# Kernel optimization log

Hardware: AMD Instinct MI355X
Metric: run time of the kernel (lower is better)

Reference implementation:

```python
import jax, jax.numpy as jnp
import numpy as np
import math

B, N, R = 1024, 50, 1000
N_POIS = 50000
D = 128
K_T = 64
K_D = 64
T_MAX = 10080.0
D_MAX = 200.0
EARTH_RADIUS_KM = 6371.0
DEG2RAD = math.pi / 180.0


def _interp_scalar(table, x):
    # Linear interpolation into 1-D table [K]; x are bin positions in [0, K-1].
    K = table.shape[0]
    x = jnp.clip(x, 0.0, K - 1 - 1e-06)
    k = jnp.floor(x).astype(jnp.int32)
    frac = x - k.astype(x.dtype)
    return (1.0 - frac) * table[k] + frac * table[jnp.minimum(k + 1, K - 1)]


def _haversine_km(lat1, lon1, lat2, lon2):
    dlat = (lat2 - lat1) * DEG2RAD
    dlon = (lon2 - lon1) * DEG2RAD
    a = jnp.sin(dlat / 2) ** 2 + jnp.cos(lat1 * DEG2RAD) * jnp.cos(lat2 * DEG2RAD) * jnp.sin(dlon / 2) ** 2
    a = jnp.clip(a, 0.0, 1.0)
    return EARTH_RADIUS_KM * 2.0 * jnp.arcsin(jnp.sqrt(a))


def setup_inputs() -> dict:
    key = jax.random.key(0)
    ks = jax.random.split(key, 16)
    poi_idx = jax.random.randint(ks[0], (B, N), 0, N_POIS)
    hour_of_week = jax.random.randint(ks[1], (B, N), 0, 169)
    lat = jax.random.uniform(ks[2], (B, N), jnp.float32)  # ~1 degree spread => up to ~150 km pairwise
    lon = jax.random.uniform(ks[3], (B, N), jnp.float32)
    t_min = jax.random.uniform(ks[4], (B, N), jnp.float32) * T_MAX
    region_centroids = jax.random.uniform(ks[5], (R, 2), jnp.float32)
    poi_emb = 0.02 * jax.random.normal(ks[6], (N_POIS + 1, D), jnp.float32)
    poi_emb = poi_emb.at[N_POIS].set(0.0)  # padding row
    time_emb = 0.02 * jax.random.normal(ks[7], (169, D), jnp.float32)
    time_emb = time_emb.at[0].set(0.0)  # padding row
    E_t = 0.1 * jax.random.normal(ks[8], (K_T,), jnp.float32)
    E_d = 0.1 * jax.random.normal(ks[9], (K_D,), jnp.float32)
    E_d_match = 0.1 * jax.random.normal(ks[10], (K_D,), jnp.float32)
    region_emb = 0.02 * jax.random.normal(ks[11], (R, D), jnp.float32)
    Wq = jax.random.normal(ks[12], (D, D), jnp.float32) / math.sqrt(D)
    Wk = jax.random.normal(ks[13], (D, D), jnp.float32) / math.sqrt(D)
    Wv = jax.random.normal(ks[14], (D, D), jnp.float32) / math.sqrt(D)
    return dict(poi_idx=poi_idx, hour_of_week=hour_of_week, lat=lat, lon=lon, t_min=t_min,
                region_centroids=region_centroids, poi_emb=poi_emb, time_emb=time_emb,
                E_t=E_t, E_d=E_d, E_d_match=E_d_match, region_emb=region_emb,
                Wq=Wq, Wk=Wk, Wv=Wv)


def reference(poi_idx, hour_of_week, lat, lon, t_min, region_centroids,
              poi_emb, time_emb, E_t, E_d, E_d_match, region_emb, Wq, Wk, Wv):
    pad_mask = poi_idx < 0  # [B, n]
    poi_safe = jnp.where(pad_mask, N_POIS, poi_idx)
    hour_safe = jnp.where(pad_mask, 0, hour_of_week)
    x = poi_emb[poi_safe] + time_emb[hour_safe]  # [B, n, D]

    # pairwise trajectory intervals [B, n, n]
    dt = jnp.abs(t_min[:, :, None] - t_min[:, None, :])
    dd = _haversine_km(lat[:, :, None], lon[:, :, None], lat[:, None, :], lon[:, None, :])
    valid = (~pad_mask).astype(x.dtype)
    valid_pair = valid[:, :, None] * valid[:, None, :]
    dt = dt * valid_pair
    dd = dd * valid_pair

    # _PairwiseBias: scalar table interpolation bias
    t_bin = jnp.clip(dt, 0.0, T_MAX) / T_MAX * (K_T - 1)
    d_bin = jnp.clip(dd, 0.0, D_MAX) / D_MAX * (K_D - 1)
    bias = _interp_scalar(E_t, t_bin) + _interp_scalar(E_d, d_bin)  # [B, n, n]

    # _SelfAttn (single head, no LN/residual, dropout=0)
    Q = x @ Wq.T
    K_ = x @ Wk.T
    V = x @ Wv.T
    scores = jnp.einsum('bnd,bmd->bnm', Q, K_) / math.sqrt(D) + bias
    scores = jnp.where(pad_mask[:, None, :], -jnp.inf, scores)
    attn = jnp.nan_to_num(jax.nn.softmax(scores, axis=-1), nan=0.0)
    S = attn @ V  # [B, n, D]

    # _MatchingLayer
    cand_lat = region_centroids[:, 0]
    cand_lon = region_centroids[:, 1]
    dd_m = _haversine_km(lat[:, :, None], lon[:, :, None], cand_lat[None, None, :], cand_lon[None, None, :])  # [B, n, R]
    dbin_m = jnp.clip(dd_m, 0.0, D_MAX) / D_MAX * (K_D - 1)
    bias_match = _interp_scalar(E_d_match, dbin_m)
    m_scores = jnp.einsum('bnd,rd->bnr', S, region_emb) / math.sqrt(D) + bias_match
    m_scores = jnp.where(pad_mask[:, :, None], -jnp.inf, m_scores)
    m_attn = jnp.nan_to_num(jax.nn.softmax(m_scores, axis=1), nan=0.0)  # softmax over trajectory dim
    scores_safe = jnp.where(pad_mask[:, :, None], 0.0, m_scores)
    return jnp.sum(m_attn * scores_safe, axis=1)  # [B, R]
```

## Files before the change

### kernel.cpp

```cpp
#include <hip/hip_runtime.h>
#include <hip/hip_bf16.h>
#include <math.h>

constexpr int BB    = 1024;
constexpr int NN    = 50;
constexpr int RR    = 1000;
constexpr int DD    = 128;
constexpr int NPOIS = 50000;
#define DEG2RADF  0.017453292519943295f
#define KHALF     0.008726646259971648f
#define RSQRTD    0.08838834764831845f
#define DBIN_C0   4013.7373f
#define DBIN_C1   668.95621f
#define TBIN_SC   0.00625f
#define PENAL     -1.0e30f

typedef __attribute__((ext_vector_type(8))) short bfrag8;
typedef __attribute__((ext_vector_type(4))) float f32x4;

__device__ __forceinline__ int swz128(int row, int k) {
    return row * 128 + ((((k) >> 3) ^ (row & 7)) << 3) + (k & 7);
}
__device__ __forceinline__ int swz64(int row, int k) {
    return row * 64 + ((((k) >> 3) ^ (row & 7)) << 3) + (k & 7);
}

__device__ __forceinline__ unsigned short f2bf(float x) {
    union { __hip_bfloat16 h; unsigned short u; } cv;
    cv.h = __float2bfloat16(x);
    return cv.u;
}

__device__ __forceinline__ float cos_small(float x) {
    float x2 = x * x;
    return 1.0f - 0.5f * x2 + 0.041666667f * x2 * x2;
}

__global__ void prep_mg(const float* __restrict__ Wq, const float* __restrict__ Wk,
                        const float* __restrict__ Wv, const float* __restrict__ Re,
                        unsigned short* __restrict__ Mt, unsigned short* __restrict__ G) {
    int k = threadIdx.x;
    if (blockIdx.x < DD) {
        int c = blockIdx.x;
        float s0 = 0.f, s1 = 0.f, s2 = 0.f, s3 = 0.f;
        for (int d = 0; d < DD; d += 4) {
            s0 += Wq[(d + 0) * DD + k] * Wk[(d + 0) * DD + c];
            s1 += Wq[(d + 1) * DD + k] * Wk[(d + 1) * DD + c];
            s2 += Wq[(d + 2) * DD + k] * Wk[(d + 2) * DD + c];
            s3 += Wq[(d + 3) * DD + k] * Wk[(d + 3) * DD + c];
        }
        Mt[c * DD + k] = f2bf((s0 + s1 + s2 + s3) * RSQRTD);
    } else {
        int r = blockIdx.x - DD;
        float s0 = 0.f, s1 = 0.f, s2 = 0.f, s3 = 0.f;
        for (int d = 0; d < DD; d += 4) {
            s0 += Wv[(d + 0) * DD + k] * Re[r * DD + d + 0];
            s1 += Wv[(d + 1) * DD + k] * Re[r * DD + d + 1];
            s2 += Wv[(d + 2) * DD + k] * Re[r * DD + d + 2];
            s3 += Wv[(d + 3) * DD + k] * Re[r * DD + d + 3];
        }
        G[r * DD + k] = f2bf((s0 + s1 + s2 + s3) * RSQRTD);
    }
}

__global__ __launch_bounds__(256) void stan_attn(
    const int* __restrict__ poi_idx, const int* __restrict__ hourw,
    const float* __restrict__ lat, const float* __restrict__ lon,
    const float* __restrict__ tmin,
    const float* __restrict__ poi_emb, const float* __restrict__ time_emb,
    const float* __restrict__ Et_g, const float* __restrict__ Ed_g,
    const unsigned short* __restrict__ Mtb, unsigned short* __restrict__ Zw) {
    __shared__ short xs[64 * 128];
    __shared__ union {
        short ys[64 * 128];
        short ps[64 * 64];
    } u2;
    __shared__ float2 Et2[64], Ed2[64];
    __shared__ float4 bnfo[64];
    __shared__ float  jpen[64];

    const int b = blockIdx.x, tid = threadIdx.x;
    const int wid = tid >> 6, lane = tid & 63;
    const int quad = lane >> 4, colr = lane & 15;

    if (tid < 64) {
        int kk = tid > 62 ? 62 : tid;
        Et2[tid] = make_float2(Et_g[kk], Et_g[kk + 1]);
        Ed2[tid] = make_float2(Ed_g[kk], Ed_g[kk + 1]);
        if (tid < NN) {
            int p = poi_idx[b * NN + tid];
            float la = lat[b * NN + tid], lo = lon[b * NN + tid];
            bnfo[tid] = make_float4(la * KHALF, lo * KHALF,
                                    cos_small(la * DEG2RADF),
                                    tmin[b * NN + tid] * TBIN_SC);
            jpen[tid] = (p < 0) ? PENAL : 0.f;
        } else {
            bnfo[tid] = make_float4(0.f, 0.f, 1.f, 0.f);
            jpen[tid] = PENAL;
        }
    }
    __syncthreads();

    for (int idx = tid; idx < 64 * 64; idx += 256) {
        int n = idx >> 6, c2 = idx & 63;
        float2 v = make_float2(0.f, 0.f);
        if (n < NN) {
            int p = poi_idx[b * NN + n];
            int pd = (p < 0);
            int ps_ = pd ? NPOIS : p;
            int hs  = pd ? 0 : hourw[b * NN + n];
            float2 pe = ((const float2*)(poi_emb  + (size_t)ps_ * DD))[c2];
            float2 te = ((const float2*)(time_emb + (size_t)hs  * DD))[c2];
            v = make_float2(pe.x + te.x, pe.y + te.y);
        }
        unsigned pack = (unsigned)f2bf(v.x) | ((unsigned)f2bf(v.y) << 16);
        ((unsigned*)xs)[n * 64 + (((c2 >> 2) ^ (n & 7)) << 2) + (c2 & 3)] = pack;
    }
    __syncthreads();

    {
        f32x4 accY[2][4];
        #pragma unroll
        for (int ct = 0; ct < 2; ct++)
            #pragma unroll
            for (int mt = 0; mt < 4; mt++) accY[ct][mt] = (f32x4){0.f, 0.f, 0.f, 0.f};
        #pragma unroll
        for (int ks = 0; ks < 4; ks++) {
            const int k0 = ks * 32 + quad * 8;
            bfrag8 av[4], bv[2];
            #pragma unroll
            for (int mt = 0; mt < 4; mt++)
                av[mt] = *(const bfrag8*)(&xs[swz128(mt * 16 + colr, k0)]);
            #pragma unroll
            for (int ct = 0; ct < 2; ct++) {
                int c = wid * 32 + ct * 16 + colr;
                bv[ct] = *(const bfrag8*)(Mtb + (size_t)c * DD + k0);
            }
            #pragma unroll
            for (int ct = 0; ct < 2; ct++)
                #pragma unroll
                for (int mt = 0; mt < 4; mt++)
                    accY[ct][mt] = __builtin_amdgcn_mfma_f32_16x16x32_bf16(
                        av[mt], bv[ct], accY[ct][mt], 0, 0, 0);
        }
        #pragma unroll
        for (int ct = 0; ct < 2; ct++)
            #pragma unroll
            for (int mt = 0; mt < 4; mt++)
                #pragma unroll
                for (int reg = 0; reg < 4; reg++) {
                    int m = mt * 16 + quad * 4 + reg;
                    int c = wid * 32 + ct * 16 + colr;
                    u2.ys[swz128(m, c)] = (short)f2bf(accY[ct][mt][reg]);
                }
    }
    __syncthreads();

    const int i = wid * 16 + colr;
    f32x4 accS[4];
    #pragma unroll
    for (int mt = 0; mt < 4; mt++) accS[mt] = (f32x4){0.f, 0.f, 0.f, 0.f};
    #pragma unroll
    for (int ks = 0; ks < 4; ks++) {
        const int k0 = ks * 32 + quad * 8;
        bfrag8 bv = *(const bfrag8*)(&u2.ys[swz128(i, k0)]);
        #pragma unroll
        for (int mt = 0; mt < 4; mt++) {
            bfrag8 av = *(const bfrag8*)(&xs[swz128(mt * 16 + colr, k0)]);
            accS[mt] = __builtin_amdgcn_mfma_f32_16x16x32_bf16(
                av, bv, accS[mt], 0, 0, 0);
        }
    }
    __syncthreads();

    {
        const float4 bi = bnfo[i];
        float sv[16];
        #pragma unroll
        for (int mt = 0; mt < 4; mt++) {
            #pragma unroll
            for (int reg = 0; reg < 4; reg++) {
                int j = mt * 16 + quad * 4 + reg;
                float4 bj = bnfo[j];
                float tb = fabsf(bi.w - bj.w);
                int   kt = (int)tb;
                float ft = tb - (float)kt;
                float2 et = Et2[kt];
                float bt = fmaf(ft, et.y - et.x, et.x);
                float du = bi.x - bj.x, dv = bi.y - bj.y;
                float a = fmaf((bi.z * bj.z) * dv, dv, du * du);
                float x = __builtin_amdgcn_sqrtf(a);
                float db = x * fmaf(a, DBIN_C1, DBIN_C0);
                int   kd = (int)db;
                float fd = db - (float)kd;
                float2 ed = Ed2[kd];
                float bd = fmaf(fd, ed.y - ed.x, ed.x);
                sv[mt * 4 + reg] = (accS[mt][reg] + bt) + (bd + jpen[j]);
            }
        }
        float mx = sv[0];
        #pragma unroll
        for (int t = 1; t < 16; t++) mx = fmaxf(mx, sv[t]);
        mx = fmaxf(mx, __shfl_xor(mx, 16, 64));
        mx = fmaxf(mx, __shfl_xor(mx, 32, 64));
        float l = 0.f;
        #pragma unroll
        for (int t = 0; t < 16; t++) {
            float p = __expf(sv[t] - mx);
            sv[t] = p;
            l += p;
        }
        l += __shfl_xor(l, 16, 64);
        l += __shfl_xor(l, 32, 64);
        float rl = __builtin_amdgcn_rcpf(l);
        #pragma unroll
        for (int mt = 0; mt < 4; mt++)
            #pragma unroll
            for (int rp = 0; rp < 2; rp++) {
                int j0 = mt * 16 + quad * 4 + rp * 2;
                unsigned lo = f2bf(sv[mt * 4 + rp * 2]     * rl);
                unsigned hi = f2bf(sv[mt * 4 + rp * 2 + 1] * rl);
                ((unsigned*)u2.ps)[i * 32 + (((j0 >> 3) ^ (i & 7)) << 2) + ((j0 & 7) >> 1)]
                    = lo | (hi << 16);
            }
    }
    __syncthreads();

    {
        f32x4 accZ[2][4];
        #pragma unroll
        for (int nt = 0; nt < 2; nt++)
            #pragma unroll
            for (int mt = 0; mt < 4; mt++) accZ[nt][mt] = (f32x4){0.f, 0.f, 0.f, 0.f};
        union BF { unsigned u[4]; bfrag8 v; };
        #pragma unroll
        for (int ks = 0; ks < 2; ks++) {
            const int k0 = ks * 32 + quad * 8;
            bfrag8 av[4];
            #pragma unroll
            for (int mt = 0; mt < 4; mt++)
                av[mt] = *(const bfrag8*)(&u2.ps[swz64(mt * 16 + colr, k0)]);
            BF bvx[2];
            #pragma unroll
            for (int nt = 0; nt < 2; nt++) {
                int d = wid * 32 + nt * 16 + colr;
                #pragma unroll
                for (int t2 = 0; t2 < 4; t2++) {
                    unsigned lo = (unsigned short)xs[swz128(k0 + 2 * t2,     d)];
                    unsigned hi = (unsigned short)xs[swz128(k0 + 2 * t2 + 1, d)];
                    bvx[nt].u[t2] = lo | (hi << 16);
                }
            }
            #pragma unroll
            for (int nt = 0; nt < 2; nt++)
                #pragma unroll
                for (int mt = 0; mt < 4; mt++)
                    accZ[nt][mt] = __builtin_amdgcn_mfma_f32_16x16x32_bf16(
                        av[mt], bvx[nt].v, accZ[nt][mt], 0, 0, 0);
        }
        unsigned short* Zb = Zw + (size_t)b * NN * DD;
        #pragma unroll
        for (int mt = 0; mt < 4; mt++)
            #pragma unroll
            for (int reg = 0; reg < 4; reg++) {
                int ii = mt * 16 + quad * 4 + reg;
                if (ii < NN) {
                    #pragma unroll
                    for (int nt = 0; nt < 2; nt++) {
                        int d = wid * 32 + nt * 16 + colr;
                        Zb[(size_t)ii * DD + d] = f2bf(accZ[nt][mt][reg]);
                    }
                }
            }
    }
}

__global__ __launch_bounds__(256) void stan_match(
    const unsigned short* __restrict__ Zw, const unsigned short* __restrict__ G,
    const float* __restrict__ cent, const float* __restrict__ Em_g,
    const int* __restrict__ poi_idx,
    const float* __restrict__ lat, const float* __restrict__ lon,
    float* __restrict__ out) {
    __shared__ short  As[64 * 128];
    __shared__ short  Bs[64 * 128];
    __shared__ float2 Em2[64];
    __shared__ float4 Rnfo[64];
    __shared__ float4 bnfo[64];

    const int tid = threadIdx.x;
    const int b = blockIdx.x, rt = blockIdx.y;
    const int rbase = rt * 64;

    if (tid < 64) {
        int kk = tid > 62 ? 62 : tid;
        Em2[tid] = make_float2(Em_g[kk], Em_g[kk + 1]);
        int rc = rbase + tid; if (rc > RR - 1) rc = RR - 1;
        float la = cent[rc * 2], lo = cent[rc * 2 + 1];
        Rnfo[tid] = make_float4(la * KHALF, lo * KHALF, cos_small(la * DEG2RADF), 0.f);
        if (tid < NN) {
            float bla = lat[b * NN + tid], blo = lon[b * NN + tid];
            float pen = (poi_idx[b * NN + tid] < 0) ? PENAL : 0.f;
            bnfo[tid] = make_float4(bla * KHALF, blo * KHALF,
                                    cos_small(bla * DEG2RADF), pen);
        } else {
            bnfo[tid] = make_float4(0.f, 0.f, 1.f, PENAL);
        }
    }
    {
        const int row = tid >> 2;
        uint4 z4 = make_uint4(0, 0, 0, 0);
        uint4 a0 = z4, a1 = z4, a2 = z4, a3 = z4;
        if (row < NN) {
            const uint4* src = (const uint4*)(Zw + (size_t)b * NN * DD + row * DD
                                              + (tid & 3) * 32);
            a0 = src[0]; a1 = src[1]; a2 = src[2]; a3 = src[3];
        }
        const int jb = (tid & 3) * 4, rx = row & 7;
        uint4* dstA = (uint4*)As;
        dstA[row * 16 + ((jb + 0) ^ rx)] = a0;
        dstA[row * 16 + ((jb + 1) ^ rx)] = a1;
        dstA[row * 16 + ((jb + 2) ^ rx)] = a2;
        dstA[row * 16 + ((jb + 3) ^ rx)] = a3;
        int gr = rbase + row; if (gr > RR - 1) gr = RR - 1;
        const uint4* srcB = (const uint4*)(G + (size_t)gr * DD + (tid & 3) * 32);
        uint4* dstB = (uint4*)Bs;
        dstB[row * 16 + ((jb + 0) ^ rx)] = srcB[0];
        dstB[row * 16 + ((jb + 1) ^ rx)] = srcB[1];
        dstB[row * 16 + ((jb + 2) ^ rx)] = srcB[2];
        dstB[row * 16 + ((jb + 3) ^ rx)] = srcB[3];
    }
    __syncthreads();

    const int wid  = tid >> 6, lane = tid & 63;
    const int quad = lane >> 4, colr = lane & 15;
    const int rL   = wid * 16 + colr;
    const int r    = rbase + rL;

    f32x4 acc[4];
    #pragma unroll
    for (int mt = 0; mt < 4; mt++) acc[mt] = (f32x4){0.f, 0.f, 0.f, 0.f};

    #pragma unroll
    for (int ks = 0; ks < 4; ks++) {
        const int k0 = ks * 32 + quad * 8;
        bfrag8 bf = *(const bfrag8*)(&Bs[swz128(rL, k0)]);
        #pragma unroll
        for (int mt = 0; mt < 4; mt++) {
            bfrag8 af = *(const bfrag8*)(&As[swz128(mt * 16 + colr, k0)]);
            acc[mt] = __builtin_amdgcn_mfma_f32_16x16x32_bf16(af, bf, acc[mt], 0, 0, 0);
        }
    }

    const float4 rv = Rnfo[rL];
    float s[16];
    #pragma unroll
    for (int mt = 0; mt < 4; mt++) {
        #pragma unroll
        for (int reg = 0; reg < 4; reg++) {
            int n = mt * 16 + quad * 4 + reg;
            float4 bn = bnfo[n];
            float du = bn.x - rv.x, dv = bn.y - rv.y;
            float a = fmaf((bn.z * rv.z) * dv, dv, du * du);
            float x = __builtin_amdgcn_sqrtf(a);
            float db = x * fmaf(a, DBIN_C1, DBIN_C0);
            int   kd = (int)db;
            float fd = db - (float)kd;
            float2 ed = Em2[kd];
            float bias = fmaf(fd, ed.y - ed.x, ed.x);
            s[mt * 4 + reg] = (acc[mt][reg] + bias) + bn.w;
        }
    }
    float m = s[0];
    #pragma unroll
    for (int t = 1; t < 16; t++) m = fmaxf(m, s[t]);
    m = fmaxf(m, __shfl_xor(m, 16, 64));
    m = fmaxf(m, __shfl_xor(m, 32, 64));
    float l = 0.f, a = 0.f;
    #pragma unroll
    for (int t = 0; t < 16; t++) {
        float p = __expf(s[t] - m);
        l += p;
        a = fmaf(p, s[t], a);
    }
    l += __shfl_xor(l, 16, 64); a += __shfl_xor(a, 16, 64);
    l += __shfl_xor(l, 32, 64); a += __shfl_xor(a, 32, 64);
    if (quad == 0 && r < RR)
        out[(size_t)b * RR + r] = a * __builtin_amdgcn_rcpf(l);
}

extern "C" void kernel_launch(void* const* d_in, const int* in_sizes, int n_in,
                              void* d_out, int out_size, void* d_ws, size_t ws_size,
                              hipStream_t stream) {
    const int*   poi_idx  = (const int*)d_in[0];
    const int*   hourw    = (const int*)d_in[1];
    const float* lat      = (const float*)d_in[2];
    const float* lon      = (const float*)d_in[3];
    const float* tmin     = (const float*)d_in[4];
    const float* cent     = (const float*)d_in[5];
    const float* poi_emb  = (const float*)d_in[6];
    const float* time_emb = (const float*)d_in[7];
    const float* E_t      = (const float*)d_in[8];
    const float* E_d      = (const float*)d_in[9];
    const float* E_dm     = (const float*)d_in[10];
    const float* Remb     = (const float*)d_in[11];
    const float* Wq       = (const float*)d_in[12];
    const float* Wk       = (const float*)d_in[13];
    const float* Wv       = (const float*)d_in[14];
    float* out            = (float*)d_out;

    unsigned short* Mtb = (unsigned short*)d_ws;
    unsigned short* Gb  = Mtb + DD * DD;
    unsigned short* Zw  = Gb + (size_t)RR * DD;

    prep_mg<<<dim3(DD + RR), DD, 0, stream>>>(Wq, Wk, Wv, Remb, Mtb, Gb);
    stan_attn<<<dim3(BB), 256, 0, stream>>>(poi_idx, hourw, lat, lon, tmin,
                                            poi_emb, time_emb, E_t, E_d, Mtb, Zw);
    stan_match<<<dim3(BB, 16), 256, 0, stream>>>(Zw, Gb, cent, E_dm, poi_idx, lat, lon, out);
}
```

Before: 189.3 us.

## Fuse attention and matching kernels with double-buffered G tiles and bpermute lookups

Merges the attention kernel and the matching kernel into one kernel per batch. The per-batch Z tile now stays in shared memory instead of round-tripping through global workspace. Inside, the kernel loops over all 16 region tiles, double-buffering the G rows with register prefetch. The E_t/E_d/E_dm table lookups are replaced with cross-lane ds_bpermute from per-lane registers instead of LDS tables. The trade-off is far less grid parallelism (1024 blocks instead of 1024x16) and a serialized loop over region tiles, plus larger LDS use that may lower occupancy.

```diff
diff --git a/kernel.cpp b/kernel.cpp
--- a/kernel.cpp
+++ b/kernel.cpp
@@ -36,6 +36,14 @@
     return 1.0f - 0.5f * x2 + 0.041666667f * x2 * x2;
 }
 
+__device__ __forceinline__ float interp_bp(float eA, float eB, float pos) {
+    int   k = (int)pos;
+    float f = pos - (float)k;
+    float lo = __int_as_float(__builtin_amdgcn_ds_bpermute(k << 2, __float_as_int(eA)));
+    float hi = __int_as_float(__builtin_amdgcn_ds_bpermute(k << 2, __float_as_int(eB)));
+    return fmaf(f, hi - lo, lo);
+}
+
 __global__ void prep_mg(const float* __restrict__ Wq, const float* __restrict__ Wk,
                         const float* __restrict__ Wv, const float* __restrict__ Re,
                         unsigned short* __restrict__ Mt, unsigned short* __restrict__ G) {
@@ -63,19 +71,21 @@
     }
 }
 
-__global__ __launch_bounds__(256) void stan_attn(
+__global__ __launch_bounds__(256) void stan_fused(
     const int* __restrict__ poi_idx, const int* __restrict__ hourw,
     const float* __restrict__ lat, const float* __restrict__ lon,
     const float* __restrict__ tmin,
     const float* __restrict__ poi_emb, const float* __restrict__ time_emb,
     const float* __restrict__ Et_g, const float* __restrict__ Ed_g,
-    const unsigned short* __restrict__ Mtb, unsigned short* __restrict__ Zw) {
+    const float* __restrict__ Em_g, const float* __restrict__ cent,
+    const unsigned short* __restrict__ Mtb, const unsigned short* __restrict__ G,
+    float* __restrict__ out) {
     __shared__ short xs[64 * 128];
     __shared__ union {
         short ys[64 * 128];
         short ps[64 * 64];
     } u2;
-    __shared__ float2 Et2[64], Ed2[64];
+    __shared__ short Bs[2][64 * 128];
     __shared__ float4 bnfo[64];
     __shared__ float  jpen[64];
 
@@ -83,10 +93,12 @@
     const int wid = tid >> 6, lane = tid & 63;
     const int quad = lane >> 4, colr = lane & 15;
 
+    const int lp1 = lane < 63 ? lane + 1 : 63;
+    const float etA = Et_g[lane], etB = Et_g[lp1];
+    const float edA = Ed_g[lane], edB = Ed_g[lp1];
+    const float emA = Em_g[lane], emB = Em_g[lp1];
+
     if (tid < 64) {
-        int kk = tid > 62 ? 62 : tid;
-        Et2[tid] = make_float2(Et_g[kk], Et_g[kk + 1]);
-        Ed2[tid] = make_float2(Ed_g[kk], Ed_g[kk + 1]);
         if (tid < NN) {
             int p = poi_idx[b * NN + tid];
             float la = lat[b * NN + tid], lo = lon[b * NN + tid];
@@ -182,19 +194,11 @@
             for (int reg = 0; reg < 4; reg++) {
                 int j = mt * 16 + quad * 4 + reg;
                 float4 bj = bnfo[j];
-                float tb = fabsf(bi.w - bj.w);
-                int   kt = (int)tb;
-                float ft = tb - (float)kt;
-                float2 et = Et2[kt];
-                float bt = fmaf(ft, et.y - et.x, et.x);
+                float bt = interp_bp(etA, etB, fabsf(bi.w - bj.w));
                 float du = bi.x - bj.x, dv = bi.y - bj.y;
                 float a = fmaf((bi.z * bj.z) * dv, dv, du * du);
                 float x = __builtin_amdgcn_sqrtf(a);
-                float db = x * fmaf(a, DBIN_C1, DBIN_C0);
-                int   kd = (int)db;
-                float fd = db - (float)kd;
-                float2 ed = Ed2[kd];
-                float bd = fmaf(fd, ed.y - ed.x, ed.x);
+                float bd = interp_bp(edA, edB, x * fmaf(a, DBIN_C1, DBIN_C0));
                 sv[mt * 4 + reg] = (accS[mt][reg] + bt) + (bd + jpen[j]);
             }
         }
@@ -226,12 +230,12 @@
     }
     __syncthreads();
 
-    {
-        f32x4 accZ[2][4];
-        #pragma unroll
-        for (int nt = 0; nt < 2; nt++)
-            #pragma unroll
-            for (int mt = 0; mt < 4; mt++) accZ[nt][mt] = (f32x4){0.f, 0.f, 0.f, 0.f};
+    f32x4 accZ[2][4];
+    #pragma unroll
+    for (int nt = 0; nt < 2; nt++)
+        #pragma unroll
+        for (int mt = 0; mt < 4; mt++) accZ[nt][mt] = (f32x4){0.f, 0.f, 0.f, 0.f};
+    {
         union BF { unsigned u[4]; bfrag8 v; };
         #pragma unroll
         for (int ks = 0; ks < 2; ks++) {
@@ -258,134 +262,119 @@
                     accZ[nt][mt] = __builtin_amdgcn_mfma_f32_16x16x32_bf16(
                         av[mt], bvx[nt].v, accZ[nt][mt], 0, 0, 0);
         }
-        unsigned short* Zb = Zw + (size_t)b * NN * DD;
+    }
+    __syncthreads();
+
+    uint4 g4;
+    const int grow = tid >> 2, gcol = (tid & 3) * 32;
+    {
+        int gr0 = grow; if (gr0 > RR - 1) gr0 = RR - 1;
+        g4 = *(const uint4*)(G + (size_t)gr0 * DD + gcol);
         #pragma unroll
         for (int mt = 0; mt < 4; mt++)
             #pragma unroll
             for (int reg = 0; reg < 4; reg++) {
-                int ii = mt * 16 + quad * 4 + reg;
-                if (ii < NN) {
-                    #pragma unroll
-                    for (int nt = 0; nt < 2; nt++) {
-                        int d = wid * 32 + nt * 16 + colr;
-                        Zb[(size_t)ii * DD + d] = f2bf(accZ[nt][mt][reg]);
-                    }
+                int zi = mt * 16 + quad * 4 + reg;
+                #pragma unroll
+                for (int nt = 0; nt < 2; nt++) {
+                    int d = wid * 32 + nt * 16 + colr;
+                    xs[swz128(zi, d)] = (short)f2bf(accZ[nt][mt][reg]);
                 }
             }
     }
-}
-
-__global__ __launch_bounds__(256) void stan_match(
-    const unsigned short* __restrict__ Zw, const unsigned short* __restrict__ G,
-    const float* __restrict__ cent, const float* __restrict__ Em_g,
-    const int* __restrict__ poi_idx,
-    const float* __restrict__ lat, const float* __restrict__ lon,
-    float* __restrict__ out) {
-    __shared__ short  As[64 * 128];
-    __shared__ short  Bs[64 * 128];
-    __shared__ float2 Em2[64];
-    __shared__ float4 Rnfo[64];
-    __shared__ float4 bnfo[64];
-
-    const int tid = threadIdx.x;
-    const int b = blockIdx.x, rt = blockIdx.y;
-    const int rbase = rt * 64;
-
-    if (tid < 64) {
-        int kk = tid > 62 ? 62 : tid;
-        Em2[tid] = make_float2(Em_g[kk], Em_g[kk + 1]);
-        int rc = rbase + tid; if (rc > RR - 1) rc = RR - 1;
-        float la = cent[rc * 2], lo = cent[rc * 2 + 1];
-        Rnfo[tid] = make_float4(la * KHALF, lo * KHALF, cos_small(la * DEG2RADF), 0.f);
-        if (tid < NN) {
-            float bla = lat[b * NN + tid], blo = lon[b * NN + tid];
-            float pen = (poi_idx[b * NN + tid] < 0) ? PENAL : 0.f;
-            bnfo[tid] = make_float4(bla * KHALF, blo * KHALF,
-                                    cos_small(bla * DEG2RADF), pen);
-        } else {
-            bnfo[tid] = make_float4(0.f, 0.f, 1.f, PENAL);
-        }
-    }
-    {
-        const int row = tid >> 2;
-        uint4 z4 = make_uint4(0, 0, 0, 0);
-        uint4 a0 = z4, a1 = z4, a2 = z4, a3 = z4;
-        if (row < NN) {
-            const uint4* src = (const uint4*)(Zw + (size_t)b * NN * DD + row * DD
-                                              + (tid & 3) * 32);
-            a0 = src[0]; a1 = src[1]; a2 = src[2]; a3 = src[3];
-        }
-        const int jb = (tid & 3) * 4, rx = row & 7;
-        uint4* dstA = (uint4*)As;
-        dstA[row * 16 + ((jb + 0) ^ rx)] = a0;
-        dstA[row * 16 + ((jb + 1) ^ rx)] = a1;
-        dstA[row * 16 + ((jb + 2) ^ rx)] = a2;
-        dstA[row * 16 + ((jb + 3) ^ rx)] = a3;
-        int gr = rbase + row; if (gr > RR - 1) gr = RR - 1;
-        const uint4* srcB = (const uint4*)(G + (size_t)gr * DD + (tid & 3) * 32);
-        uint4* dstB = (uint4*)Bs;
-        dstB[row * 16 + ((jb + 0) ^ rx)] = srcB[0];
-        dstB[row * 16 + ((jb + 1) ^ rx)] = srcB[1];
-        dstB[row * 16 + ((jb + 2) ^ rx)] = srcB[2];
-        dstB[row * 16 + ((jb + 3) ^ rx)] = srcB[3];
-    }
-    __syncthreads();
-
-    const int wid  = tid >> 6, lane = tid & 63;
-    const int quad = lane >> 4, colr = lane & 15;
-    const int rL   = wid * 16 + colr;
-    const int r    = rbase + rL;
-
-    f32x4 acc[4];
+    float bnx[16], bny[16], bnz[16], pen[16];
     #pragma unroll
-    for (int mt = 0; mt < 4; mt++) acc[mt] = (f32x4){0.f, 0.f, 0.f, 0.f};
-
-    #pragma unroll
-    for (int ks = 0; ks < 4; ks++) {
-        const int k0 = ks * 32 + quad * 8;
-        bfrag8 bf = *(const bfrag8*)(&Bs[swz128(rL, k0)]);
-        #pragma unroll
-        for (int mt = 0; mt < 4; mt++) {
-            bfrag8 af = *(const bfrag8*)(&As[swz128(mt * 16 + colr, k0)]);
-            acc[mt] = __builtin_amdgcn_mfma_f32_16x16x32_bf16(af, bf, acc[mt], 0, 0, 0);
-        }
-    }
-
-    const float4 rv = Rnfo[rL];
-    float s[16];
-    #pragma unroll
-    for (int mt = 0; mt < 4; mt++) {
+    for (int mt = 0; mt < 4; mt++)
         #pragma unroll
         for (int reg = 0; reg < 4; reg++) {
             int n = mt * 16 + quad * 4 + reg;
             float4 bn = bnfo[n];
-            float du = bn.x - rv.x, dv = bn.y - rv.y;
-            float a = fmaf((bn.z * rv.z) * dv, dv, du * du);
+            bnx[mt * 4 + reg] = bn.x; bny[mt * 4 + reg] = bn.y;
+            bnz[mt * 4 + reg] = bn.z; pen[mt * 4 + reg] = jpen[n];
+        }
+    {
+        const int jb = (tid & 3) * 4, rx = grow & 7;
+        ((uint4*)Bs[0])[grow * 16 + (jb ^ rx)] = g4;
+    }
+    uint4 g4b, g4c, g4d;
+    {
+        int gr0 = grow; if (gr0 > RR - 1) gr0 = RR - 1;
+        const uint4* src = (const uint4*)(G + (size_t)gr0 * DD + gcol);
+        g4b = src[1]; g4c = src[2]; g4d = src[3];
+        const int jb = (tid & 3) * 4, rx = grow & 7;
+        uint4* dst = (uint4*)Bs[0];
+        dst[grow * 16 + ((jb + 1) ^ rx)] = g4b;
+        dst[grow * 16 + ((jb + 2) ^ rx)] = g4c;
+        dst[grow * 16 + ((jb + 3) ^ rx)] = g4d;
+    }
+    __syncthreads();
+
+    const int rL = wid * 16 + colr;
+    for (int rt = 0; rt < 16; rt++) {
+        const int cur = rt & 1;
+        uint4 n0, n1, n2, n3;
+        if (rt < 15) {
+            int gr = (rt + 1) * 64 + grow; if (gr > RR - 1) gr = RR - 1;
+            const uint4* src = (const uint4*)(G + (size_t)gr * DD + gcol);
+            n0 = src[0]; n1 = src[1]; n2 = src[2]; n3 = src[3];
+        }
+
+        f32x4 acc[4];
+        #pragma unroll
+        for (int mt = 0; mt < 4; mt++) acc[mt] = (f32x4){0.f, 0.f, 0.f, 0.f};
+        #pragma unroll
+        for (int ks = 0; ks < 4; ks++) {
+            const int k0 = ks * 32 + quad * 8;
+            bfrag8 bf = *(const bfrag8*)(&Bs[cur][swz128(rL, k0)]);
+            #pragma unroll
+            for (int mt = 0; mt < 4; mt++) {
+                bfrag8 af = *(const bfrag8*)(&xs[swz128(mt * 16 + colr, k0)]);
+                acc[mt] = __builtin_amdgcn_mfma_f32_16x16x32_bf16(af, bf, acc[mt], 0, 0, 0);
+            }
+        }
+
+        const int r = rt * 64 + rL;
+        int rc = r > RR - 1 ? RR - 1 : r;
+        float2 cc = ((const float2*)cent)[rc];
+        const float rvx = cc.x * KHALF, rvy = cc.y * KHALF;
+        const float rvz = cos_small(cc.x * DEG2RADF);
+
+        float s[16];
+        #pragma unroll
+        for (int t = 0; t < 16; t++) {
+            float du = bnx[t] - rvx, dv = bny[t] - rvy;
+            float a = fmaf((bnz[t] * rvz) * dv, dv, du * du);
             float x = __builtin_amdgcn_sqrtf(a);
-            float db = x * fmaf(a, DBIN_C1, DBIN_C0);
-            int   kd = (int)db;
-            float fd = db - (float)kd;
-            float2 ed = Em2[kd];
-            float bias = fmaf(fd, ed.y - ed.x, ed.x);
-            s[mt * 4 + reg] = (acc[mt][reg] + bias) + bn.w;
-        }
-    }
-    float m = s[0];
-    #pragma unroll
-    for (int t = 1; t < 16; t++) m = fmaxf(m, s[t]);
-    m = fmaxf(m, __shfl_xor(m, 16, 64));
-    m = fmaxf(m, __shfl_xor(m, 32, 64));
-    float l = 0.f, a = 0.f;
-    #pragma unroll
-    for (int t = 0; t < 16; t++) {
-        float p = __expf(s[t] - m);
-        l += p;
-        a = fmaf(p, s[t], a);
-    }
-    l += __shfl_xor(l, 16, 64); a += __shfl_xor(a, 16, 64);
-    l += __shfl_xor(l, 32, 64); a += __shfl_xor(a, 32, 64);
-    if (quad == 0 && r < RR)
-        out[(size_t)b * RR + r] = a * __builtin_amdgcn_rcpf(l);
+            float bias = interp_bp(emA, emB, x * fmaf(a, DBIN_C1, DBIN_C0));
+            s[t] = (acc[t >> 2][t & 3] + bias) + pen[t];
+        }
+        float m = s[0];
+        #pragma unroll
+        for (int t = 1; t < 16; t++) m = fmaxf(m, s[t]);
+        m = fmaxf(m, __shfl_xor(m, 16, 64));
+        m = fmaxf(m, __shfl_xor(m, 32, 64));
+        float l = 0.f, a = 0.f;
+        #pragma unroll
+        for (int t = 0; t < 16; t++) {
+            float p = __expf(s[t] - m);
+            l += p;
+            a = fmaf(p, s[t], a);
+        }
+        l += __shfl_xor(l, 16, 64); a += __shfl_xor(a, 16, 64);
+        l += __shfl_xor(l, 32, 64); a += __shfl_xor(a, 32, 64);
+        if (quad == 0 && r < RR)
+            out[(size_t)b * RR + r] = a * __builtin_amdgcn_rcpf(l);
+
+        if (rt < 15) {
+            const int jb = (tid & 3) * 4, rx = grow & 7;
+            uint4* dst = (uint4*)Bs[cur ^ 1];
+            dst[grow * 16 + ((jb + 0) ^ rx)] = n0;
+            dst[grow * 16 + ((jb + 1) ^ rx)] = n1;
+            dst[grow * 16 + ((jb + 2) ^ rx)] = n2;
+            dst[grow * 16 + ((jb + 3) ^ rx)] = n3;
+        }
+        __syncthreads();
+    }
 }
 
 extern "C" void kernel_launch(void* const* d_in, const int* in_sizes, int n_in,
@@ -410,10 +399,9 @@
 
     unsigned short* Mtb = (unsigned short*)d_ws;
     unsigned short* Gb  = Mtb + DD * DD;
-    unsigned short* Zw  = Gb + (size_t)RR * DD;
 
     prep_mg<<<dim3(DD + RR), DD, 0, stream>>>(Wq, Wk, Wv, Remb, Mtb, Gb);
-    stan_attn<<<dim3(BB), 256, 0, stream>>>(poi_idx, hourw, lat, lon, tmin,
-                                            poi_emb, time_emb, E_t, E_d, Mtb, Zw);
-    stan_match<<<dim3(BB, 16), 256, 0, stream>>>(Zw, Gb, cent, E_dm, poi_idx, lat, lon, out);
-}
+    stan_fused<<<dim3(BB), 256, 0, stream>>>(poi_idx, hourw, lat, lon, tmin,
+                                             poi_emb, time_emb, E_t, E_d, E_dm,
+                                             cent, Mtb, Gb, out);
+}
```

Measured after the change: 212.9 us. +12.5%, slower.

## Use ds_bpermute register-table interpolation and stronger LDS swizzle

Applied to the files above, without the earlier changes.

Replaces the shared-memory float2 lookup tables for the time and distance bias interpolation with per-lane register copies of the tables, read through ds_bpermute cross-lane shuffles. This removes the LDS table arrays and the random-index LDS loads, which can bank-conflict. The LDS swizzle now XORs row bits 3-5 into the pattern to spread bank accesses further. The matching kernel also loads per-row bnfo values into registers before the MFMA loop so those loads can overlap with it. Each lookup now issues two bpermutes, which still go through the LDS hardware and add some register pressure.

```diff
diff --git a/kernel.cpp b/kernel.cpp
--- a/kernel.cpp
+++ b/kernel.cpp
@@ -18,11 +18,12 @@
 typedef __attribute__((ext_vector_type(8))) short bfrag8;
 typedef __attribute__((ext_vector_type(4))) float f32x4;
 
-__device__ __forceinline__ int swz128(int row, int k) {
-    return row * 128 + ((((k) >> 3) ^ (row & 7)) << 3) + (k & 7);
-}
-__device__ __forceinline__ int swz64(int row, int k) {
-    return row * 64 + ((((k) >> 3) ^ (row & 7)) << 3) + (k & 7);
+__device__ __forceinline__ int swzS(int row) { return (row ^ (row >> 3)) & 7; }
+__device__ __forceinline__ int swzA(int row, int k) {
+    return row * 128 + (((k >> 3) ^ swzS(row)) << 3) + (k & 7);
+}
+__device__ __forceinline__ int swzP(int row, int k) {
+    return row * 64 + (((k >> 3) ^ swzS(row)) << 3) + (k & 7);
 }
 
 __device__ __forceinline__ unsigned short f2bf(float x) {
@@ -34,6 +35,14 @@
 __device__ __forceinline__ float cos_small(float x) {
     float x2 = x * x;
     return 1.0f - 0.5f * x2 + 0.041666667f * x2 * x2;
+}
+
+__device__ __forceinline__ float interp_bp(float eA, float eB, float pos) {
+    int   k = (int)pos;
+    float f = pos - (float)k;
+    float lo = __int_as_float(__builtin_amdgcn_ds_bpermute(k << 2, __float_as_int(eA)));
+    float hi = __int_as_float(__builtin_amdgcn_ds_bpermute(k << 2, __float_as_int(eB)));
+    return fmaf(f, hi - lo, lo);
 }
 
 __global__ void prep_mg(const float* __restrict__ Wq, const float* __restrict__ Wk,
@@ -75,7 +84,6 @@
         short ys[64 * 128];
         short ps[64 * 64];
     } u2;
-    __shared__ float2 Et2[64], Ed2[64];
     __shared__ float4 bnfo[64];
     __shared__ float  jpen[64];
 
@@ -83,10 +91,11 @@
     const int wid = tid >> 6, lane = tid & 63;
     const int quad = lane >> 4, colr = lane & 15;
 
+    const int lp1 = lane < 63 ? lane + 1 : 63;
+    const float etA = Et_g[lane], etB = Et_g[lp1];
+    const float edA = Ed_g[lane], edB = Ed_g[lp1];
+
     if (tid < 64) {
-        int kk = tid > 62 ? 62 : tid;
-        Et2[tid] = make_float2(Et_g[kk], Et_g[kk + 1]);
-        Ed2[tid] = make_float2(Ed_g[kk], Ed_g[kk + 1]);
         if (tid < NN) {
             int p = poi_idx[b * NN + tid];
             float la = lat[b * NN + tid], lo = lon[b * NN + tid];
@@ -114,7 +123,7 @@
             v = make_float2(pe.x + te.x, pe.y + te.y);
         }
         unsigned pack = (unsigned)f2bf(v.x) | ((unsigned)f2bf(v.y) << 16);
-        ((unsigned*)xs)[n * 64 + (((c2 >> 2) ^ (n & 7)) << 2) + (c2 & 3)] = pack;
+        ((unsigned*)xs)[n * 64 + (((c2 >> 2) ^ swzS(n)) << 2) + (c2 & 3)] = pack;
     }
     __syncthreads();
 
@@ -130,7 +139,7 @@
             bfrag8 av[4], bv[2];
             #pragma unroll
             for (int mt = 0; mt < 4; mt++)
-                av[mt] = *(const bfrag8*)(&xs[swz128(mt * 16 + colr, k0)]);
+                av[mt] = *(const bfrag8*)(&xs[swzA(mt * 16 + colr, k0)]);
             #pragma unroll
             for (int ct = 0; ct < 2; ct++) {
                 int c = wid * 32 + ct * 16 + colr;
@@ -151,7 +160,7 @@
                 for (int reg = 0; reg < 4; reg++) {
                     int m = mt * 16 + quad * 4 + reg;
                     int c = wid * 32 + ct * 16 + colr;
-                    u2.ys[swz128(m, c)] = (short)f2bf(accY[ct][mt][reg]);
+                    u2.ys[swzA(m, c)] = (short)f2bf(accY[ct][mt][reg]);
                 }
     }
     __syncthreads();
@@ -163,10 +172,10 @@
     #pragma unroll
     for (int ks = 0; ks < 4; ks++) {
         const int k0 = ks * 32 + quad * 8;
-        bfrag8 bv = *(const bfrag8*)(&u2.ys[swz128(i, k0)]);
+        bfrag8 bv = *(const bfrag8*)(&u2.ys[swzA(i, k0)]);
         #pragma unroll
         for (int mt = 0; mt < 4; mt++) {
-            bfrag8 av = *(const bfrag8*)(&xs[swz128(mt * 16 + colr, k0)]);
+            bfrag8 av = *(const bfrag8*)(&xs[swzA(mt * 16 + colr, k0)]);
             accS[mt] = __builtin_amdgcn_mfma_f32_16x16x32_bf16(
                 av, bv, accS[mt], 0, 0, 0);
         }
@@ -182,19 +191,11 @@
             for (int reg = 0; reg < 4; reg++) {
                 int j = mt * 16 + quad * 4 + reg;
                 float4 bj = bnfo[j];
-                float tb = fabsf(bi.w - bj.w);
-                int   kt = (int)tb;
-                float ft = tb - (float)kt;
-                float2 et = Et2[kt];
-                float bt = fmaf(ft, et.y - et.x, et.x);
+                float bt = interp_bp(etA, etB, fabsf(bi.w - bj.w));
                 float du = bi.x - bj.x, dv = bi.y - bj.y;
                 float a = fmaf((bi.z * bj.z) * dv, dv, du * du);
                 float x = __builtin_amdgcn_sqrtf(a);
-                float db = x * fmaf(a, DBIN_C1, DBIN_C0);
-                int   kd = (int)db;
-                float fd = db - (float)kd;
-                float2 ed = Ed2[kd];
-                float bd = fmaf(fd, ed.y - ed.x, ed.x);
+                float bd = interp_bp(edA, edB, x * fmaf(a, DBIN_C1, DBIN_C0));
                 sv[mt * 4 + reg] = (accS[mt][reg] + bt) + (bd + jpen[j]);
             }
         }
@@ -220,7 +221,7 @@
                 int j0 = mt * 16 + quad * 4 + rp * 2;
                 unsigned lo = f2bf(sv[mt * 4 + rp * 2]     * rl);
                 unsigned hi = f2bf(sv[mt * 4 + rp * 2 + 1] * rl);
-                ((unsigned*)u2.ps)[i * 32 + (((j0 >> 3) ^ (i & 7)) << 2) + ((j0 & 7) >> 1)]
+                ((unsigned*)u2.ps)[i * 32 + (((j0 >> 3) ^ swzS(i)) << 2) + ((j0 & 7) >> 1)]
                     = lo | (hi << 16);
             }
     }
@@ -239,15 +240,15 @@
             bfrag8 av[4];
             #pragma unroll
             for (int mt = 0; mt < 4; mt++)
-                av[mt] = *(const bfrag8*)(&u2.ps[swz64(mt * 16 + colr, k0)]);
+                av[mt] = *(const bfrag8*)(&u2.ps[swzP(mt * 16 + colr, k0)]);
             BF bvx[2];
             #pragma unroll
             for (int nt = 0; nt < 2; nt++) {
                 int d = wid * 32 + nt * 16 + colr;
                 #pragma unroll
                 for (int t2 = 0; t2 < 4; t2++) {
-                    unsigned lo = (unsigned short)xs[swz128(k0 + 2 * t2,     d)];
-                    unsigned hi = (unsigned short)xs[swz128(k0 + 2 * t2 + 1, d)];
+                    unsigned lo = (unsigned short)xs[swzA(k0 + 2 * t2,     d)];
+                    unsigned hi = (unsigned short)xs[swzA(k0 + 2 * t2 + 1, d)];
                     bvx[nt].u[t2] = lo | (hi << 16);
                 }
             }
@@ -283,7 +284,6 @@
     float* __restrict__ out) {
     __shared__ short  As[64 * 128];
     __shared__ short  Bs[64 * 128];
-    __shared__ float2 Em2[64];
     __shared__ float4 Rnfo[64];
     __shared__ float4 bnfo[64];
 
@@ -291,9 +291,11 @@
     const int b = blockIdx.x, rt = blockIdx.y;
     const int rbase = rt * 64;
 
+    const int lane = tid & 63;
+    const int lp1 = lane < 63 ? lane + 1 : 63;
+    const float emA = Em_g[lane], emB = Em_g[lp1];
+
     if (tid < 64) {
-        int kk = tid > 62 ? 62 : tid;
-        Em2[tid] = make_float2(Em_g[kk], Em_g[kk + 1]);
         int rc = rbase + tid; if (rc > RR - 1) rc = RR - 1;
         float la = cent[rc * 2], lo = cent[rc * 2 + 1];
         Rnfo[tid] = make_float4(la * KHALF, lo * KHALF, cos_small(la * DEG2RADF), 0.f);
@@ -315,7 +317,7 @@
                                               + (tid & 3) * 32);
             a0 = src[0]; a1 = src[1]; a2 = src[2]; a3 = src[3];
         }
-        const int jb = (tid & 3) * 4, rx = row & 7;
+        const int jb = (tid & 3) * 4, rx = swzS(row);
         uint4* dstA = (uint4*)As;
         dstA[row * 16 + ((jb + 0) ^ rx)] = a0;
         dstA[row * 16 + ((jb + 1) ^ rx)] = a1;
@@ -331,11 +333,21 @@
     }
     __syncthreads();
 
-    const int wid  = tid >> 6, lane = tid & 63;
+    const int wid  = tid >> 6;
     const int quad = lane >> 4, colr = lane & 15;
     const int rL   = wid * 16 + colr;
     const int r    = rbase + rL;
 
+    float bnx[16], bny[16], bnz[16], pen[16];
+    #pragma unroll
+    for (int mt = 0; mt < 4; mt++)
+        #pragma unroll
+        for (int reg = 0; reg < 4; reg++) {
+            float4 bn = bnfo[mt * 16 + quad * 4 + reg];
+            bnx[mt * 4 + reg] = bn.x; bny[mt * 4 + reg] = bn.y;
+            bnz[mt * 4 + reg] = bn.z; pen[mt * 4 + reg] = bn.w;
+        }
+
     f32x4 acc[4];
     #pragma unroll
     for (int mt = 0; mt < 4; mt++) acc[mt] = (f32x4){0.f, 0.f, 0.f, 0.f};
@@ -343,10 +355,10 @@
     #pragma unroll
     for (int ks = 0; ks < 4; ks++) {
         const int k0 = ks * 32 + quad * 8;
-        bfrag8 bf = *(const bfrag8*)(&Bs[swz128(rL, k0)]);
+        bfrag8 bf = *(const bfrag8*)(&Bs[swzA(rL, k0)]);
         #pragma unroll
         for (int mt = 0; mt < 4; mt++) {
-            bfrag8 af = *(const bfrag8*)(&As[swz128(mt * 16 + colr, k0)]);
+            bfrag8 af = *(const bfrag8*)(&As[swzA(mt * 16 + colr, k0)]);
             acc[mt] = __builtin_amdgcn_mfma_f32_16x16x32_bf16(af, bf, acc[mt], 0, 0, 0);
         }
     }
@@ -354,21 +366,12 @@
     const float4 rv = Rnfo[rL];
     float s[16];
     #pragma unroll
-    for (int mt = 0; mt < 4; mt++) {
-        #pragma unroll
-        for (int reg = 0; reg < 4; reg++) {
-            int n = mt * 16 + quad * 4 + reg;
-            float4 bn = bnfo[n];
-            float du = bn.x - rv.x, dv = bn.y - rv.y;
-            float a = fmaf((bn.z * rv.z) * dv, dv, du * du);
-            float x = __builtin_amdgcn_sqrtf(a);
-            float db = x * fmaf(a, DBIN_C1, DBIN_C0);
-            int   kd = (int)db;
-            float fd = db - (float)kd;
-            float2 ed = Em2[kd];
-            float bias = fmaf(fd, ed.y - ed.x, ed.x);
-            s[mt * 4 + reg] = (acc[mt][reg] + bias) + bn.w;
-        }
+    for (int t = 0; t < 16; t++) {
+        float du = bnx[t] - rv.x, dv = bny[t] - rv.y;
+        float a = fmaf((bnz[t] * rv.z) * dv, dv, du * du);
+        float x = __builtin_amdgcn_sqrtf(a);
+        float bias = interp_bp(emA, emB, x * fmaf(a, DBIN_C1, DBIN_C0));
+        s[t] = (acc[t >> 2][t & 3] + bias) + pen[t];
     }
     float m = s[0];
     #pragma unroll
```

Result: slower. 217.3 us (+14.8%).
